# Kernel optimization log

Measured on AMD Instinct MI355X. Metric: run time of the kernel, lower is better.

Reference implementation:

```python
import jax, jax.numpy as jnp
import numpy as np
from jax import lax

B, S, T, H, VIN, VOUT = 32, 128, 64, 512, 32000, 32000
PAD_IDX = 1


def setup_inputs() -> dict:
    key = jax.random.key(0)
    ks = jax.random.split(key, 20)
    sc = 0.05
    rn = lambda k, shp: (jax.random.normal(k, shp, jnp.float32) * sc)
    return {
        "src": jax.random.randint(ks[0], (B, S), 0, VIN),
        "src_len": jnp.full((B,), S, dtype=jnp.int32),
        "trg": jax.random.randint(ks[1], (B, T), 0, VOUT),
        "enc_emb": rn(ks[2], (VIN, H)),
        "enc_wih": rn(ks[3], (4 * H, H)),
        "enc_whh": rn(ks[4], (4 * H, H)),
        "enc_bih": rn(ks[5], (4 * H,)),
        "enc_bhh": rn(ks[6], (4 * H,)),
        "enc_fc_w": rn(ks[7], (H, H)),
        "enc_fc_b": rn(ks[8], (H,)),
        "dec_emb": rn(ks[9], (VOUT, H)),
        "attn_w": rn(ks[10], (H, 2 * H)),
        "attn_b": rn(ks[11], (H,)),
        "attn_v": rn(ks[12], (H,)),
        "dec_wih": rn(ks[13], (4 * H, 2 * H)),
        "dec_whh": rn(ks[14], (4 * H, H)),
        "dec_bih": rn(ks[15], (4 * H,)),
        "dec_bhh": rn(ks[16], (4 * H,)),
        "out_w": rn(ks[17], (VOUT, 3 * H)),
        "out_b": rn(ks[18], (VOUT,)),
    }


def _lstm_cell(x, h, c, wih, whh, bih, bhh):
    # PyTorch gate order: i, f, g, o
    g = x @ wih.T + bih + h @ whh.T + bhh
    i, f, gg, o = jnp.split(g, 4, axis=-1)
    c = jax.nn.sigmoid(f) * c + jax.nn.sigmoid(i) * jnp.tanh(gg)
    h = jax.nn.sigmoid(o) * jnp.tanh(c)
    return h, c


def reference(src, src_len, trg, enc_emb, enc_wih, enc_whh, enc_bih, enc_bhh,
              enc_fc_w, enc_fc_b, dec_emb, attn_w, attn_b, attn_v,
              dec_wih, dec_whh, dec_bih, dec_bhh, out_w, out_b):
    b = src.shape[0]
    # ---- Encoder: single-layer LSTM over time (full lengths) ----
    emb = enc_emb[src].transpose(1, 0, 2)  # [S,B,H] time-major
    h0 = jnp.zeros((b, H), emb.dtype)
    c0 = jnp.zeros((b, H), emb.dtype)

    def enc_step(carry, x_t):
        h, c = carry
        h, c = _lstm_cell(x_t, h, c, enc_wih, enc_whh, enc_bih, enc_bhh)
        return (h, c), h

    (hf, cf), enc_out = lax.scan(enc_step, (h0, c0), emb)  # enc_out [S,B,H]
    hidden = jnp.tanh(hf @ enc_fc_w.T + enc_fc_b)  # [B,H]
    enc_bt = enc_out.transpose(1, 0, 2)  # [B,S,H]
    mask = src != PAD_IDX  # [B,S]

    # ---- Decoder: teacher forcing (ratio=1.0), scan over target steps ----
    def dec_step(carry, tok):
        h, c = carry
        e = dec_emb[tok]  # [B,H]
        # Bahdanau attention
        hrep = jnp.broadcast_to(h[:, None, :], enc_bt.shape)  # [B,S,H]
        energy = jnp.tanh(jnp.concatenate([hrep, enc_bt], -1) @ attn_w.T + attn_b)
        score = energy @ attn_v  # [B,S]
        score = jnp.where(mask, score, jnp.float32(-1e10))
        a = jax.nn.softmax(score, axis=1)
        weighted = jnp.einsum('bs,bsh->bh', a, enc_bt)  # [B,H]
        x = jnp.concatenate([e, weighted], -1)  # [B,2H]
        h, c = _lstm_cell(x, h, c, dec_wih, dec_whh, dec_bih, dec_bhh)
        pred = jnp.concatenate([h, weighted, e], -1) @ out_w.T + out_b  # [B,V]
        return (h, c), pred

    tokens = trg.T  # [T,B]
    (_, _), logits = lax.scan(dec_step, (hidden, cf), tokens[:-1])  # [T-1,B,V]
    outputs = jnp.concatenate(
        [jnp.zeros((1, b, VOUT), logits.dtype), logits], axis=0)  # [T,B,V]
    return outputs
```

## Files before the change

kernel.cpp:

```cpp
#include <hip/hip_runtime.h>

typedef unsigned short u16;
typedef unsigned int u32;
typedef unsigned long long u64;
typedef __attribute__((ext_vector_type(8))) short bf16x8;
typedef __attribute__((ext_vector_type(8))) unsigned short u16x8;
typedef __attribute__((ext_vector_type(4))) unsigned short u16x4;
typedef __attribute__((ext_vector_type(4))) float f32x4;

#define DEVI static __device__ __forceinline__
#define MFMA __builtin_amdgcn_mfma_f32_16x16x32_bf16

constexpr int B = 32, S = 128, T = 64, H = 512, V = 32000;
constexpr int H4 = 4 * H;
constexpr int TD = T - 1;
constexpr int MOUT = TD * B;
constexpr int KOUT = 3 * H;
constexpr int PAD_IDX = 1;

DEVI u16 f2bf(float f) {
  union { float f; unsigned u; } v; v.f = f;
  unsigned r = (v.u + 0x7fffu + ((v.u >> 16) & 1u)) >> 16;
  return (u16)r;
}
DEVI float bf2f(u16 h) {
  union { unsigned u; float f; } v; v.u = ((unsigned)h) << 16;
  return v.f;
}
DEVI float sigm(float x) { return 1.f / (1.f + __expf(-x)); }
DEVI float tanh_(float x) {
  float ax = fabsf(x);
  float e = __expf(-2.f * ax);
  float t = (1.f - e) / (1.f + e);
  return x < 0.f ? -t : t;
}
DEVI float tanhf_(float x) {
  float e = __expf(2.f * x);
  return 1.f - 2.f * __builtin_amdgcn_rcpf(e + 1.f);
}
DEVI int swz(int row, int k8) { return row * 32 + ((k8 ^ (row & 3)) << 3); }

DEVI u64 pack4u(const u16* p) {
  return (u64)p[0] | ((u64)p[1] << 16) | ((u64)p[2] << 32) | ((u64)p[3] << 48);
}
DEVI u64 xstore(u16* p, u64 v) {
  return __hip_atomic_exchange((u64*)p, v, __ATOMIC_RELAXED,
                               __HIP_MEMORY_SCOPE_AGENT);
}
DEVI u64 xstore64(u64* p, u64 v) {
  return __hip_atomic_exchange(p, v, __ATOMIC_RELAXED,
                               __HIP_MEMORY_SCOPE_AGENT);
}
DEVI void sstore(unsigned* p, unsigned v) {
  __hip_atomic_exchange(p, v, __ATOMIC_RELAXED, __HIP_MEMORY_SCOPE_AGENT);
}
DEVI void poll_bo(unsigned* p, unsigned tgt) {
  int it = 0;
  long long t0 = (long long)__builtin_amdgcn_s_memrealtime();
  while (__hip_atomic_load(p, __ATOMIC_RELAXED, __HIP_MEMORY_SCOPE_AGENT) <
         tgt) {
    if (it < 4) {
      __builtin_amdgcn_s_sleep(1);
      it++;
    } else {
      __builtin_amdgcn_s_sleep(4);
    }
    if ((long long)__builtin_amdgcn_s_memrealtime() - t0 > 20000000ll) break;
  }
}

__global__ __launch_bounds__(256) void gemm_bt(
    const u16* __restrict__ A, int lda,
    const u16* __restrict__ Bt, int ldb,
    float* __restrict__ C, int ldc,
    const float* __restrict__ bias, int M, int K, int bf16out) {
  __shared__ u16 As[128 * 32], Bs[128 * 32];
  const int tid = threadIdx.x;
  const int m0 = blockIdx.y * 128, n0 = blockIdx.x * 128;
  const int lane = tid & 63, w = tid >> 6, wm = w >> 1, wn = w & 1;
  const int lr = lane & 15, lk = lane >> 4;
  f32x4 acc[4][4] = {};
  const int r = tid >> 1, cc = (tid & 1) * 16, k8b = (tid & 1) * 2;

  for (int k0 = 0; k0 < K; k0 += 32) {
    {
      long gr = m0 + r;
      u16x8 v0 = {}, v1 = {};
      if (gr < M) {
        const u16* s = A + gr * (long)lda + k0 + cc;
        v0 = *(const u16x8*)s;
        v1 = *(const u16x8*)(s + 8);
      }
      *(u16x8*)&As[swz(r, k8b)] = v0;
      *(u16x8*)&As[swz(r, k8b + 1)] = v1;
    }
    {
      const u16* s = Bt + (long)(n0 + r) * ldb + k0 + cc;
      u16x8 v0 = *(const u16x8*)s;
      u16x8 v1 = *(const u16x8*)(s + 8);
      *(u16x8*)&Bs[swz(r, k8b)] = v0;
      *(u16x8*)&Bs[swz(r, k8b + 1)] = v1;
    }
    __syncthreads();
    bf16x8 af[4], bfr[4];
#pragma unroll
    for (int mi = 0; mi < 4; mi++)
      af[mi] = *(const bf16x8*)&As[swz(wm * 64 + mi * 16 + lr, lk)];
#pragma unroll
    for (int ni = 0; ni < 4; ni++)
      bfr[ni] = *(const bf16x8*)&Bs[swz(wn * 64 + ni * 16 + lr, lk)];
#pragma unroll
    for (int mi = 0; mi < 4; mi++)
#pragma unroll
      for (int ni = 0; ni < 4; ni++)
        acc[mi][ni] = MFMA(af[mi], bfr[ni], acc[mi][ni], 0, 0, 0);
    __syncthreads();
  }
#pragma unroll
  for (int ni = 0; ni < 4; ni++) {
    int col = n0 + wn * 64 + ni * 16 + lr;
    float bs = bias ? bias[col] : 0.f;
#pragma unroll
    for (int mi = 0; mi < 4; mi++) {
#pragma unroll
      for (int rr = 0; rr < 4; rr++) {
        long row = m0 + wm * 64 + mi * 16 + lk * 4 + rr;
        if (row < M) {
          float v = acc[mi][ni][rr] + bs;
          if (bf16out)
            ((u16*)C)[row * (long)ldc + col] = f2bf(v);
          else
            C[row * (long)ldc + col] = v;
        }
      }
    }
  }
}

DEVI void gemm_tile512(const u16* A, int lda, const u16* Bt, int ldb,
                       float* C, int ldc, const float* bias, int M, int K,
                       int mt, int nt) {
  __shared__ u16 As[128 * 32], Bs[128 * 32];
  const int tid = threadIdx.x;
  const bool act = tid < 256;
  const int m0 = mt * 128, n0 = nt * 128;
  const int lane = tid & 63, w = tid >> 6, wm = (w >> 1) & 1, wn = w & 1;
  const int lr = lane & 15, lk = lane >> 4;
  f32x4 acc[4][4] = {};
  const int r = (tid >> 1) & 127, cc = (tid & 1) * 16, k8b = (tid & 1) * 2;

  for (int k0 = 0; k0 < K; k0 += 32) {
    if (act) {
      {
        long gr = m0 + r;
        u16x8 v0 = {}, v1 = {};
        if (gr < M) {
          const u16* s = A + gr * (long)lda + k0 + cc;
          v0 = *(const u16x8*)s;
          v1 = *(const u16x8*)(s + 8);
        }
        *(u16x8*)&As[swz(r, k8b)] = v0;
        *(u16x8*)&As[swz(r, k8b + 1)] = v1;
      }
      {
        const u16* s = Bt + (long)(n0 + r) * ldb + k0 + cc;
        u16x8 v0 = *(const u16x8*)s;
        u16x8 v1 = *(const u16x8*)(s + 8);
        *(u16x8*)&Bs[swz(r, k8b)] = v0;
        *(u16x8*)&Bs[swz(r, k8b + 1)] = v1;
      }
    }
    __syncthreads();
    if (act) {
      bf16x8 af[4], bfr[4];
#pragma unroll
      for (int mi = 0; mi < 4; mi++)
        af[mi] = *(const bf16x8*)&As[swz(wm * 64 + mi * 16 + lr, lk)];
#pragma unroll
      for (int ni = 0; ni < 4; ni++)
        bfr[ni] = *(const bf16x8*)&Bs[swz(wn * 64 + ni * 16 + lr, lk)];
#pragma unroll
      for (int mi = 0; mi < 4; mi++)
#pragma unroll
        for (int ni = 0; ni < 4; ni++)
          acc[mi][ni] = MFMA(af[mi], bfr[ni], acc[mi][ni], 0, 0, 0);
    }
    __syncthreads();
  }
  if (act) {
#pragma unroll
    for (int ni = 0; ni < 4; ni++) {
      int col = n0 + wn * 64 + ni * 16 + lr;
      float bs = bias ? bias[col] : 0.f;
#pragma unroll
      for (int mi = 0; mi < 4; mi++) {
#pragma unroll
        for (int rr = 0; rr < 4; rr++) {
          long row = m0 + wm * 64 + mi * 16 + lk * 4 + rr;
          if (row < M) C[row * (long)ldc + col] = acc[mi][ni][rr] + bs;
        }
      }
    }
  }
}

__global__ void zero_f(float* p, long n) {
  long i = (long)blockIdx.x * 256 + threadIdx.x;
  long st = (long)gridDim.x * 256;
  for (; i < n; i += st) p[i] = 0.f;
}

__global__ void zero_u(unsigned* p, int n) {
  int i = blockIdx.x * 256 + threadIdx.x;
  if (i < n) p[i] = 0u;
}

__global__ void cast_bf(const float* __restrict__ src, u16* __restrict__ dst,
                        int ld, int off, int Csz) {
  long row = blockIdx.y;
  int col = blockIdx.x * 256 + threadIdx.x;
  dst[row * Csz + col] = f2bf(src[row * ld + off + col]);
}

__global__ void cast_perm(const float* __restrict__ src, int ld, int off,
                          u16* __restrict__ dst) {
  int np = blockIdx.y;
  int c = blockIdx.x * 256 + threadIdx.x;
  int g = np & 3, jH = np >> 2;
  dst[(size_t)np * H + c] = f2bf(src[(size_t)(g * H + jH) * ld + off + c]);
}

__global__ void pack_wdec_p(const float* __restrict__ wih,
                            const float* __restrict__ whh,
                            u16* __restrict__ dst) {
  int r = blockIdx.y;
  int k = blockIdx.x * 256 + threadIdx.x;
  int g = r & 3, j = r >> 2;
  int srow = g * H + j;
  float v = (k < 512) ? wih[(size_t)srow * (2 * H) + 512 + k]
                      : whh[(size_t)srow * H + (k - 512)];
  dst[(size_t)r * 1024 + k] = f2bf(v);
}

__global__ void bias_perm(const float* __restrict__ a,
                          const float* __restrict__ b, float* __restrict__ o) {
  int np = blockIdx.x * 256 + threadIdx.x;
  int g = np & 3, jH = np >> 2;
  int r = g * H + jH;
  o[np] = a[r] + b[r];
}

__global__ void gather_src_emb(const int* __restrict__ src,
                               const float* __restrict__ emb,
                               u16* __restrict__ dst) {
  int row = blockIdx.y;
  int t = row >> 5, b = row & 31;
  int c = blockIdx.x * 256 + threadIdx.x;
  int tok = src[b * S + t];
  dst[(long)row * H + c] = f2bf(emb[(long)tok * H + c]);
}

__global__ void gather_trg_emb(const int* __restrict__ trg,
                               const float* __restrict__ emb,
                               u16* __restrict__ xout) {
  int row = blockIdx.y;
  int t = row >> 5, b = row & 31;
  int c = blockIdx.x * 256 + threadIdx.x;
  int tok = trg[b * T + t];
  xout[(long)row * KOUT + 2 * H + c] = f2bf(emb[(long)tok * H + c]);
}

__global__ __launch_bounds__(512) void enc_fused(
    unsigned* fes, const u16* __restrict__ wenc_p,
    const float* __restrict__ xih_p, u16* hstep, u16* enc_bt_bf, float* cbuf,
    const u16* __restrict__ xoute, const u16* __restrict__ wihE_p,
    float* __restrict__ eih_p, const float* __restrict__ bdec_p,
    const float* __restrict__ out_w, u16* __restrict__ outw_bf) {
  const int bk = blockIdx.x;
  if (bk >= 288) {
    long i = (long)(bk - 288) * 512 + threadIdx.x;
    const long n4 = (long)V * KOUT / 4, st = 96L * 512;
    for (; i < n4; i += st) {
      float4 v = ((const float4*)out_w)[i];
      u16x4 o;
      o[0] = f2bf(v.x); o[1] = f2bf(v.y); o[2] = f2bf(v.z); o[3] = f2bf(v.w);
      *(u16x4*)&outw_bf[i * 4] = o;
    }
    return;
  }
  if (bk >= 32) {
    int job = bk - 32, mt = job >> 4, nt = job & 15;
    gemm_tile512(xoute, KOUT, wihE_p, H, eih_p, H4, bdec_p, MOUT, H, mt, nt);
    return;
  }
  __shared__ float gs[32][64];
  __shared__ float c_s[512];
  __shared__ u16 hx[512];
  const int tid = threadIdx.x;
  const int wave = tid >> 6, lane = tid & 63;
  const int lr = lane & 15, lk = lane >> 4;
  const int bq = tid >> 4, jl = tid & 15;
  c_s[tid] = 0.f;
  const int mt = wave & 1, nt = wave >> 1;
  const int n = nt * 16 + lr;
  bf16x8 wf[16];
  {
    const u16* wp = wenc_p + (size_t)(bk * 64 + n) * 512 + lk * 8;
#pragma unroll
    for (int kt = 0; kt < 16; kt++) wf[kt] = *(const bf16x8*)(wp + kt * 32);
  }
  for (int t = 0; t < S; t++) {
    if (t > 0 && tid < 32) poll_bo(fes + tid * 16, (unsigned)t);
    __syncthreads();
    float4 xv = *(const float4*)(xih_p + ((size_t)t * B + bq) * H4 +
                                 (bk * 16 + jl) * 4);
    {
      const u16* ab =
          hstep + (size_t)t * B * H + (size_t)(mt * 16 + lr) * H + lk * 8;
      f32x4 acc = {};
#pragma unroll
      for (int kt = 0; kt < 16; kt++) {
        bf16x8 a = *(const bf16x8*)(ab + kt * 32);
        acc = MFMA(a, wf[kt], acc, 0, 0, 0);
      }
#pragma unroll
      for (int rr = 0; rr < 4; rr++) gs[mt * 16 + lk * 4 + rr][n] = acc[rr];
    }
    __syncthreads();
    {
      float gi = xv.x + gs[bq][jl * 4 + 0];
      float gf = xv.y + gs[bq][jl * 4 + 1];
      float gg = xv.z + gs[bq][jl * 4 + 2];
      float go = xv.w + gs[bq][jl * 4 + 3];
      float cn = sigm(gf) * c_s[tid] + sigm(gi) * tanh_(gg);
      c_s[tid] = cn;
      u16 h16 = f2bf(sigm(go) * tanh_(cn));
      hx[tid] = h16;
      enc_bt_bf[((size_t)bq * S + t) * H + bk * 16 + jl] = h16;
    }
    __syncthreads();
    u64 kp = 0;
    if (tid < 128) {
      int bb = tid >> 2, q = tid & 3;
      kp = xstore(hstep + (size_t)(t + 1) * B * H + (size_t)bb * H + bk * 16 +
                      q * 4,
                  pack4u(&hx[bb * 16 + q * 4]));
    }
    if (wave < 2) {
      asm volatile("" :: "v"(kp));
      asm volatile("s_waitcnt vmcnt(0)" ::: "memory");
    }
    __syncthreads();
    if (tid == 0) sstore(fes + bk * 16, (unsigned)(t + 1));
  }
  cbuf[bq * H + bk * 16 + jl] = c_s[tid];
}

__global__ __launch_bounds__(512) void dec_persist32(
    unsigned* fhs, unsigned* fws, unsigned* fps, const float* __restrict__ fc_w,
    const float* __restrict__ fc_b, const u16* __restrict__ wdec_p,
    const u16* __restrict__ a1_bf, const float* __restrict__ attn_v,
    const int* __restrict__ src, const u16* __restrict__ hf_bf,
    const float* __restrict__ cbuf, const u16* __restrict__ epart_bf,
    const u16* __restrict__ enc_bt_bf, const float* __restrict__ eih_p,
    u16* hstep, u16* wstep, float* hpstep, u16* __restrict__ xout_bf) {
  __shared__ float buf[8][512];
  __shared__ float hps[512];
  __shared__ float hp2[32][16];
  __shared__ float gh[32][64];
  __shared__ float gw[32][64];
  __shared__ float sc[128], red[2];
  __shared__ int smask[128];
  __shared__ float c_s[512];
  __shared__ u16 hx[512];
  const int tid = threadIdx.x, bk = blockIdx.x;
  const int wave = tid >> 6, lane = tid & 63;
  const int lr = lane & 15, lk = lane >> 4;
  const int bq = tid >> 4, jl = tid & 15;
  c_s[tid] = cbuf[bq * H + bk * 16 + jl];
  if (tid < 128) smask[tid] = src[bk * S + tid];
  float av8[8];
#pragma unroll
  for (int e = 0; e < 8; e++) av8[e] = attn_v[lane * 8 + e];
  if (wave < 2) {
    const u16* ab = hf_bf + (size_t)(wave * 16 + lr) * H + lk * 8;
    const float* frow = fc_w + (size_t)(bk * 16 + lr) * H + lk * 8;
    f32x4 acc = {};
#pragma unroll
    for (int kt = 0; kt < 16; kt++) {
      bf16x8 a = *(const bf16x8*)(ab + kt * 32);
      bf16x8 w;
#pragma unroll
      for (int e = 0; e < 8; e++) w[e] = (short)f2bf(frow[kt * 32 + e]);
      acc = MFMA(a, w, acc, 0, 0, 0);
    }
    float bs = fc_b[bk * 16 + lr];
#pragma unroll
    for (int rr = 0; rr < 4; rr++)
      hx[(wave * 16 + lk * 4 + rr) * 16 + lr] = f2bf(tanh_(acc[rr] + bs));
  }
  __syncthreads();
  {
    u64 kp = 0;
    if (tid < 128) {
      int bb = tid >> 2, q = tid & 3;
      kp = xstore(hstep + (size_t)bb * H + bk * 16 + q * 4,
                  pack4u(&hx[bb * 16 + q * 4]));
    }
    if (wave < 2) {
      asm volatile("" :: "v"(kp));
      asm volatile("s_waitcnt vmcnt(0)" ::: "memory");
    }
    __syncthreads();
    if (tid == 0) sstore(fhs + bk * 16, 1u);
  }
  const int mt = wave & 1, nt = wave >> 1;
  const int n = nt * 16 + lr;
  const u16* wpw = wdec_p + (size_t)(bk * 64 + n) * 1024 + lk * 8;
  const u16* wph = wpw + 512;
  bf16x8 wwf[16];
#pragma unroll
  for (int kt = 0; kt < 16; kt++) wwf[kt] = *(const bf16x8*)(wpw + kt * 32);
  for (int t = 0; t < TD; t++) {
    if (tid < 32) poll_bo(fhs + tid * 16, (unsigned)(t + 1));
    __syncthreads();
    float4 xv = *(const float4*)(eih_p + ((size_t)t * B + bq) * H4 +
                                 (bk * 16 + jl) * 4);
    {
      const u16* ah =
          hstep + (size_t)t * B * H + (size_t)(mt * 16 + lr) * H + lk * 8;
      f32x4 acc = {};
#pragma unroll
      for (int kt = 0; kt < 16; kt++) {
        bf16x8 a = *(const bf16x8*)(ah + kt * 32);
        bf16x8 w = *(const bf16x8*)(wph + kt * 32);
        acc = MFMA(a, w, acc, 0, 0, 0);
      }
#pragma unroll
      for (int rr = 0; rr < 4; rr++) gh[mt * 16 + lk * 4 + rr][n] = acc[rr];
    }
    if (wave < 2) {
      const u16* ah =
          hstep + (size_t)t * B * H + (size_t)(wave * 16 + lr) * H + lk * 8;
      const u16* bp = a1_bf + (size_t)(bk * 16 + lr) * 512 + lk * 8;
      f32x4 acc = {};
#pragma unroll
      for (int kt = 0; kt < 16; kt++) {
        bf16x8 a = *(const bf16x8*)(ah + kt * 32);
        bf16x8 w = *(const bf16x8*)(bp + kt * 32);
        acc = MFMA(a, w, acc, 0, 0, 0);
      }
#pragma unroll
      for (int rr = 0; rr < 4; rr++)
        hp2[wave * 16 + lk * 4 + rr][lr] = acc[rr];
    }
    __syncthreads();
    {
      u64 kp = 0;
      if (tid < 256) {
        int b = tid >> 3, ql = tid & 7;
        u64 pk = (u64)__float_as_uint(hp2[b][ql * 2]) |
                 ((u64)__float_as_uint(hp2[b][ql * 2 + 1]) << 32);
        kp = xstore64(
            (u64*)(hpstep + ((size_t)t * B + b) * 512 + bk * 16 + ql * 2), pk);
      }
      if (wave < 4) {
        asm volatile("" :: "v"(kp));
        asm volatile("s_waitcnt vmcnt(0)" ::: "memory");
      }
      __syncthreads();
      if (tid == 0) sstore(fps + bk * 16, (unsigned)(t + 1));
    }
    if (tid < 32) poll_bo(fps + tid * 16, (unsigned)(t + 1));
    __syncthreads();
    hps[tid] = hpstep[((size_t)t * B + bk) * 512 + tid];
    __syncthreads();
    {
      const int j0 = lane * 8;
      float hp8[8];
#pragma unroll
      for (int e = 0; e < 8; e++) hp8[e] = hps[j0 + e];
#pragma unroll 4
      for (int i = 0; i < 16; i++) {
        int s = wave * 16 + i;
        u16x8 ep = *(const u16x8*)&epart_bf[((size_t)bk * S + s) * H + j0];
        float a = 0.f;
#pragma unroll
        for (int e = 0; e < 8; e++) a += av8[e] * tanhf_(hp8[e] + bf2f(ep[e]));
#pragma unroll
        for (int o = 32; o; o >>= 1) a += __shfl_xor(a, o);
        if (lane == 0) sc[s] = (smask[s] == PAD_IDX) ? -1e10f : a;
      }
    }
    __syncthreads();
    if (tid < 64) {
      float v = fmaxf(sc[tid], sc[tid + 64]);
#pragma unroll
      for (int o = 32; o; o >>= 1) v = fmaxf(v, __shfl_xor(v, o));
      if (tid == 0) red[0] = v;
    }
    __syncthreads();
    if (tid < 64) {
      float mx = red[0];
      float e0 = __expf(sc[tid] - mx), e1 = __expf(sc[tid + 64] - mx);
      sc[tid] = e0;
      sc[tid + 64] = e1;
      float v = e0 + e1;
#pragma unroll
      for (int o = 32; o; o >>= 1) v += __shfl_xor(v, o);
      if (tid == 0) red[1] = 1.f / v;
    }
    __syncthreads();
    {
      float acc8[8] = {};
      const int j0 = lane * 8;
#pragma unroll 4
      for (int i = 0; i < 16; i++) {
        int s = wave * 16 + i;
        float ps = sc[s];
        u16x8 ev = *(const u16x8*)&enc_bt_bf[((size_t)bk * S + s) * H + j0];
#pragma unroll
        for (int e = 0; e < 8; e++) acc8[e] += ps * bf2f(ev[e]);
      }
#pragma unroll
      for (int e = 0; e < 8; e++) buf[wave][j0 + e] = acc8[e];
    }
    __syncthreads();
    {
      u64 kp = 0;
      if (tid < 128) {
        float inv = red[1];
        int j0 = tid * 4;
        u16x4 o;
#pragma unroll
        for (int i = 0; i < 4; i++) {
          float wj = (buf[0][j0 + i] + buf[1][j0 + i] + buf[2][j0 + i] +
                      buf[3][j0 + i] + buf[4][j0 + i] + buf[5][j0 + i] +
                      buf[6][j0 + i] + buf[7][j0 + i]) *
                     inv;
          o[i] = f2bf(wj);
        }
        *(u16x4*)&xout_bf[((size_t)t * B + bk) * KOUT + H + j0] = o;
        u64 val = (u64)o[0] | ((u64)o[1] << 16) | ((u64)o[2] << 32) |
                  ((u64)o[3] << 48);
        kp = xstore(wstep + ((size_t)t * B + bk) * H + j0, val);
      }
      if (wave < 2) {
        asm volatile("" :: "v"(kp));
        asm volatile("s_waitcnt vmcnt(0)" ::: "memory");
      }
      __syncthreads();
      if (tid == 0) sstore(fws + bk * 16, (unsigned)(t + 1));
    }
    if (tid < 32) poll_bo(fws + tid * 16, (unsigned)(t + 1));
    __syncthreads();
    {
      const u16* aw =
          wstep + (size_t)t * B * H + (size_t)(mt * 16 + lr) * H + lk * 8;
      f32x4 acc = {};
#pragma unroll
      for (int kt = 0; kt < 16; kt++) {
        bf16x8 a = *(const bf16x8*)(aw + kt * 32);
        acc = MFMA(a, wwf[kt], acc, 0, 0, 0);
      }
#pragma unroll
      for (int rr = 0; rr < 4; rr++) gw[mt * 16 + lk * 4 + rr][n] = acc[rr];
    }
    __syncthreads();
    {
      float gi = xv.x + gh[bq][jl * 4 + 0] + gw[bq][jl * 4 + 0];
      float gf = xv.y + gh[bq][jl * 4 + 1] + gw[bq][jl * 4 + 1];
      float gg = xv.z + gh[bq][jl * 4 + 2] + gw[bq][jl * 4 + 2];
      float go = xv.w + gh[bq][jl * 4 + 3] + gw[bq][jl * 4 + 3];
      float cn = sigm(gf) * c_s[tid] + sigm(gi) * tanh_(gg);
      c_s[tid] = cn;
      u16 h16 = f2bf(sigm(go) * tanh_(cn));
      hx[tid] = h16;
      xout_bf[((size_t)t * B + bq) * KOUT + bk * 16 + jl] = h16;
    }
    __syncthreads();
    {
      u64 kp = 0;
      if (tid < 128) {
        int bb = tid >> 2, q = tid & 3;
        kp = xstore(hstep + (size_t)(t + 1) * B * H + (size_t)bb * H +
                        bk * 16 + q * 4,
                    pack4u(&hx[bb * 16 + q * 4]));
      }
      if (wave < 2) {
        asm volatile("" :: "v"(kp));
        asm volatile("s_waitcnt vmcnt(0)" ::: "memory");
      }
      __syncthreads();
      if (tid == 0) sstore(fhs + bk * 16, (unsigned)(t + 2));
    }
  }
}

extern "C" void kernel_launch(void* const* d_in, const int* in_sizes, int n_in,
                              void* d_out, int out_size, void* d_ws,
                              size_t ws_size, hipStream_t stream) {
  const int* src = (const int*)d_in[0];
  const int* trg = (const int*)d_in[2];
  const float* enc_emb = (const float*)d_in[3];
  const float* enc_wih = (const float*)d_in[4];
  const float* enc_whh = (const float*)d_in[5];
  const float* enc_bih = (const float*)d_in[6];
  const float* enc_bhh = (const float*)d_in[7];
  const float* fc_w = (const float*)d_in[8];
  const float* fc_b = (const float*)d_in[9];
  const float* dec_emb = (const float*)d_in[10];
  const float* attn_w = (const float*)d_in[11];
  const float* attn_b = (const float*)d_in[12];
  const float* attn_v = (const float*)d_in[13];
  const float* dec_wih = (const float*)d_in[14];
  const float* dec_whh = (const float*)d_in[15];
  const float* dec_bih = (const float*)d_in[16];
  const float* dec_bhh = (const float*)d_in[17];
  const float* out_w = (const float*)d_in[18];
  const float* out_b = (const float*)d_in[19];
  float* out = (float*)d_out;

  char* wp = (char*)d_ws;
  auto alloc = [&](size_t n) {
    char* p = wp;
    wp += (n + 255) & ~(size_t)255;
    return p;
  };
  u16* outw_bf = (u16*)alloc((size_t)V * KOUT * 2);
  u16* wihenc_p = (u16*)alloc((size_t)H4 * H * 2);
  u16* wihE_p = (u16*)alloc((size_t)H4 * H * 2);
  u16* wenc_p = (u16*)alloc((size_t)H4 * H * 2);
  u16* wdec_p = (u16*)alloc((size_t)H4 * 2 * H * 2);
  u16* attnw2_bf = (u16*)alloc((size_t)H * H * 2);
  u16* a1_bf = (u16*)alloc((size_t)H * H * 2);
  u16* xemb_bf = (u16*)alloc((size_t)S * B * H * 2);
  float* xih_p = (float*)alloc((size_t)S * B * H4 * 4);
  u16* enc_bt_bf = (u16*)alloc((size_t)B * S * H * 2);
  u16* epart_bf = (u16*)alloc((size_t)B * S * H * 2);
  float* eih_p = (float*)alloc((size_t)MOUT * H4 * 4);
  u16* xout_bf = (u16*)alloc((size_t)MOUT * KOUT * 2);
  u16* hstep_enc = (u16*)alloc((size_t)(S + 1) * B * H * 2);
  u16* hstep_dec = (u16*)alloc((size_t)T * B * H * 2);
  u16* wstep = (u16*)alloc((size_t)TD * B * H * 2);
  float* hpstep = (float*)alloc((size_t)TD * B * H * 4);
  float* cbuf = (float*)alloc((size_t)B * H * 4);
  float* benc_p = (float*)alloc((size_t)H4 * 4);
  float* bdec_p = (float*)alloc((size_t)H4 * 4);
  unsigned* flags = (unsigned*)alloc(2048 * 4);
  unsigned* fes = flags;
  unsigned* fhs = flags + 512;
  unsigned* fws = flags + 1024;
  unsigned* fps = flags + 1536;

  dim3 blk(256);
  zero_f<<<dim3(256), blk, 0, stream>>>(out, (long)B * V);
  zero_u<<<dim3(8), blk, 0, stream>>>(flags, 2048);
  zero_u<<<dim3(32), blk, 0, stream>>>((unsigned*)hstep_enc, B * H / 2);
  cast_perm<<<dim3(H / 256, H4), blk, 0, stream>>>(enc_wih, H, 0, wihenc_p);
  cast_perm<<<dim3(H / 256, H4), blk, 0, stream>>>(dec_wih, 2 * H, 0, wihE_p);
  cast_perm<<<dim3(H / 256, H4), blk, 0, stream>>>(enc_whh, H, 0, wenc_p);
  pack_wdec_p<<<dim3(4, H4), blk, 0, stream>>>(dec_wih, dec_whh, wdec_p);
  cast_bf<<<dim3(H / 256, H), blk, 0, stream>>>(attn_w, attnw2_bf, 2 * H, H, H);
  cast_bf<<<dim3(H / 256, H), blk, 0, stream>>>(attn_w, a1_bf, 2 * H, 0, H);
  bias_perm<<<dim3(H4 / 256), blk, 0, stream>>>(enc_bih, enc_bhh, benc_p);
  bias_perm<<<dim3(H4 / 256), blk, 0, stream>>>(dec_bih, dec_bhh, bdec_p);
  gather_src_emb<<<dim3(H / 256, S * B), blk, 0, stream>>>(src, enc_emb,
                                                           xemb_bf);
  gather_trg_emb<<<dim3(H / 256, MOUT), blk, 0, stream>>>(trg, dec_emb,
                                                          xout_bf);
  gemm_bt<<<dim3(H4 / 128, (S * B) / 128), blk, 0, stream>>>(
      xemb_bf, H, wihenc_p, H, xih_p, H4, benc_p, S * B, H, 0);
  enc_fused<<<dim3(384), dim3(512), 0, stream>>>(
      fes, wenc_p, xih_p, hstep_enc, enc_bt_bf, cbuf, xout_bf + 2 * H, wihE_p,
      eih_p, bdec_p, out_w, outw_bf);
  gemm_bt<<<dim3(H / 128, (B * S) / 128), blk, 0, stream>>>(
      enc_bt_bf, H, attnw2_bf, H, (float*)epart_bf, H, attn_b, B * S, H, 1);
  dec_persist32<<<dim3(32), dim3(512), 0, stream>>>(
      fhs, fws, fps, fc_w, fc_b, wdec_p, a1_bf, attn_v, src,
      hstep_enc + (size_t)S * B * H, cbuf, epart_bf, enc_bt_bf, eih_p,
      hstep_dec, wstep, hpstep, xout_bf);
  gemm_bt<<<dim3(V / 128, (MOUT + 127) / 128), blk, 0, stream>>>(
      xout_bf, KOUT, outw_bf, KOUT, out + (size_t)B * V, V, out_b, MOUT, KOUT,
      0);
}
```

Before: 2.934 ms.

## Fuse output projection GEMM into persistent decoder, overlapping with recurrence via flags

```diff
diff --git a/kernel.cpp b/kernel.cpp
--- a/kernel.cpp
+++ b/kernel.cpp
@@ -65,6 +65,14 @@
     } else {
       __builtin_amdgcn_s_sleep(4);
     }
+    if ((long long)__builtin_amdgcn_s_memrealtime() - t0 > 20000000ll) break;
+  }
+}
+DEVI void poll_slow(unsigned* p, unsigned tgt) {
+  long long t0 = (long long)__builtin_amdgcn_s_memrealtime();
+  while (__hip_atomic_load(p, __ATOMIC_RELAXED, __HIP_MEMORY_SCOPE_AGENT) <
+         tgt) {
+    __builtin_amdgcn_s_sleep(16);
     if ((long long)__builtin_amdgcn_s_memrealtime() - t0 > 20000000ll) break;
   }
 }
@@ -356,14 +364,30 @@
   cbuf[bq * H + bk * 16 + jl] = c_s[tid];
 }
 
-__global__ __launch_bounds__(512) void dec_persist32(
+__global__ __launch_bounds__(512) void dec_fused(
     unsigned* fhs, unsigned* fws, unsigned* fps, const float* __restrict__ fc_w,
     const float* __restrict__ fc_b, const u16* __restrict__ wdec_p,
     const u16* __restrict__ a1_bf, const float* __restrict__ attn_v,
     const int* __restrict__ src, const u16* __restrict__ hf_bf,
     const float* __restrict__ cbuf, const u16* __restrict__ epart_bf,
     const u16* __restrict__ enc_bt_bf, const float* __restrict__ eih_p,
-    u16* hstep, u16* wstep, float* hpstep, u16* __restrict__ xout_bf) {
+    u16* hstep, u16* wstep, float* hpstep, u16* __restrict__ xout_bf,
+    const u16* __restrict__ outw_bf, const float* __restrict__ out_b,
+    float* __restrict__ out) {
+  const int tid = threadIdx.x, bk = blockIdx.x;
+  if (bk >= 32) {
+    const int g = bk - 32;
+    for (int j = g; j < 16 * 250; j += 224) {
+      int mt = j / 250, nt = j % 250;
+      int tmax = mt * 4 + 3;
+      unsigned tgt = (unsigned)((tmax > TD - 1 ? TD - 1 : tmax) + 2);
+      if (tid < 32) poll_slow(fhs + tid * 16, tgt);
+      __syncthreads();
+      gemm_tile512(xout_bf, KOUT, outw_bf, KOUT, out + (size_t)B * V, V,
+                   out_b, MOUT, KOUT, mt, nt);
+    }
+    return;
+  }
   __shared__ float buf[8][512];
   __shared__ float hps[512];
   __shared__ float hp2[32][16];
@@ -373,7 +397,6 @@
   __shared__ int smask[128];
   __shared__ float c_s[512];
   __shared__ u16 hx[512];
-  const int tid = threadIdx.x, bk = blockIdx.x;
   const int wave = tid >> 6, lane = tid & 63;
   const int lr = lane & 15, lk = lane >> 4;
   const int bq = tid >> 4, jl = tid & 15;
@@ -494,15 +517,7 @@
     }
     __syncthreads();
     if (tid < 64) {
-      float v = fmaxf(sc[tid], sc[tid + 64]);
-#pragma unroll
-      for (int o = 32; o; o >>= 1) v = fmaxf(v, __shfl_xor(v, o));
-      if (tid == 0) red[0] = v;
-    }
-    __syncthreads();
-    if (tid < 64) {
-      float mx = red[0];
-      float e0 = __expf(sc[tid] - mx), e1 = __expf(sc[tid + 64] - mx);
+      float e0 = __expf(sc[tid]), e1 = __expf(sc[tid + 64]);
       sc[tid] = e0;
       sc[tid + 64] = e1;
       float v = e0 + e1;
@@ -540,10 +555,10 @@
                      inv;
           o[i] = f2bf(wj);
         }
-        *(u16x4*)&xout_bf[((size_t)t * B + bk) * KOUT + H + j0] = o;
         u64 val = (u64)o[0] | ((u64)o[1] << 16) | ((u64)o[2] << 32) |
                   ((u64)o[3] << 48);
         kp = xstore(wstep + ((size_t)t * B + bk) * H + j0, val);
+        kp ^= xstore(&xout_bf[((size_t)t * B + bk) * KOUT + H + j0], val);
       }
       if (wave < 2) {
         asm volatile("" :: "v"(kp));
@@ -576,16 +591,18 @@
       c_s[tid] = cn;
       u16 h16 = f2bf(sigm(go) * tanh_(cn));
       hx[tid] = h16;
-      xout_bf[((size_t)t * B + bq) * KOUT + bk * 16 + jl] = h16;
     }
     __syncthreads();
     {
       u64 kp = 0;
       if (tid < 128) {
         int bb = tid >> 2, q = tid & 3;
+        u64 hv = pack4u(&hx[bb * 16 + q * 4]);
         kp = xstore(hstep + (size_t)(t + 1) * B * H + (size_t)bb * H +
                         bk * 16 + q * 4,
-                    pack4u(&hx[bb * 16 + q * 4]));
+                    hv);
+        kp ^= xstore(&xout_bf[((size_t)t * B + bb) * KOUT + bk * 16 + q * 4],
+                     hv);
       }
       if (wave < 2) {
         asm volatile("" :: "v"(kp));
@@ -676,11 +693,8 @@
       eih_p, bdec_p, out_w, outw_bf);
   gemm_bt<<<dim3(H / 128, (B * S) / 128), blk, 0, stream>>>(
       enc_bt_bf, H, attnw2_bf, H, (float*)epart_bf, H, attn_b, B * S, H, 1);
-  dec_persist32<<<dim3(32), dim3(512), 0, stream>>>(
+  dec_fused<<<dim3(256), dim3(512), 0, stream>>>(
       fhs, fws, fps, fc_w, fc_b, wdec_p, a1_bf, attn_v, src,
       hstep_enc + (size_t)S * B * H, cbuf, epart_bf, enc_bt_bf, eih_p,
-      hstep_dec, wstep, hpstep, xout_bf);
-  gemm_bt<<<dim3(V / 128, (MOUT + 127) / 128), blk, 0, stream>>>(
-      xout_bf, KOUT, outw_bf, KOUT, out + (size_t)B * V, V, out_b, MOUT, KOUT,
-      0);
-}
+      hstep_dec, wstep, hpstep, xout_bf, outw_bf, out_b, out);
+}
```

After: 2.815 ms. -4.1%, faster.
